# Optimization experiments

Measured on AMD Instinct MI355X. Metric: run time of the kernel, lower is better.

The kernel has to match this reference:

```python
import jax, jax.numpy as jnp
import numpy as np

N = 100_000        # PPI nodes
F_IN = 512         # num_features
H1, H2 = 16, 32    # GCN hidden / out channels
E = 3_200_000      # edges
NUM_DRUGS = 1024
B = 4096           # DDI batch rows


def setup_inputs() -> dict:
    key = jax.random.key(0)
    ks = jax.random.split(key, 16)
    s = 0.05
    return {
        "x": jax.random.normal(ks[0], (N, F_IN), jnp.float32),
        "edge_index": jax.random.randint(ks[1], (2, E), 0, N, dtype=jnp.int64),
        "DDI_feature": jax.random.normal(ks[2], (B, NUM_DRUGS + H2), jnp.float32),
        "W1": jax.random.normal(ks[3], (F_IN, H1), jnp.float32) * s,
        "b1": jax.random.normal(ks[4], (H1,), jnp.float32) * s,
        "W2": jax.random.normal(ks[5], (H1, H2), jnp.float32) * s,
        "b2": jax.random.normal(ks[6], (H2,), jnp.float32) * s,
        "fW1": jax.random.normal(ks[7], (NUM_DRUGS + H2, 64), jnp.float32) * s,
        "fb1": jax.random.normal(ks[8], (64,), jnp.float32) * s,
        "fW2": jax.random.normal(ks[9], (64, 16), jnp.float32) * s,
        "fb2": jax.random.normal(ks[10], (16,), jnp.float32) * s,
        "fW3": jax.random.normal(ks[11], (16, 1), jnp.float32) * s,
        "fb3": jax.random.normal(ks[12], (1,), jnp.float32) * s,
    }


def _gcn_conv(x, src, dst, W, b):
    """torch_geometric GCNConv with add_self_loops=True, symmetric norm.
    lin -> D^{-1/2} (A + I) D^{-1/2} -> + bias."""
    h = x @ W                                   # [N, out] linear first (faithful to GCNConv)
    ones = jnp.ones(src.shape[0], h.dtype)
    deg = jax.ops.segment_sum(ones, dst, num_segments=N) + 1.0  # +1 self-loop
    dinv = jax.lax.rsqrt(deg)                   # deg > 0 guaranteed by self-loop
    norm = dinv[src] * dinv[dst]                # [E]
    agg = jax.ops.segment_sum(h[src] * norm[:, None], dst, num_segments=N)
    agg = agg + h * (dinv * dinv)[:, None]      # self-loop message, norm = 1/deg
    return agg + b


def reference(x, edge_index, DDI_feature, W1, b1, W2, b2, fW1, fb1, fW2, fb2, fW3, fb3):
    src, dst = edge_index[0], edge_index[1]
    # PPI branch: conv1 -> relu -> (dropout: eval mode = identity) -> conv2 -> relu
    ppi = jax.nn.relu(_gcn_conv(x, src, dst, W1, b1))
    ppi = jax.nn.relu(_gcn_conv(ppi, src, dst, W2, b2))          # [N, 32]
    # DDI branch: fc1 -> relu -> fc2 -> relu -> fc3 -> relu
    ddi = jax.nn.relu(DDI_feature @ fW1 + fb1)
    ddi = jax.nn.relu(ddi @ fW2 + fb2)
    ddi = jax.nn.relu(ddi @ fW3 + fb3)                           # [B, 1]
    return ppi, ddi
```

## Files before the change

### kernel.cpp

```cpp
#include <hip/hip_runtime.h>

#define N_NODES 100000
#define HALF_N  50000
#define FEAT_IN 512
#define C1 16
#define C2 32
#define NEDGE 3200000
#define B_DDI 4096
#define F_DDI 1056

#define NBUCK 196
#define CAP_BUCK 32768
#define BIN_C 12288
#define NB_BIN ((NEDGE + BIN_C - 1) / BIN_C)
#define PB_CAP 12288

typedef float f4v __attribute__((ext_vector_type(4)));

#define O_DINV   0u
#define O_RP2    524288u
#define O_COL    1572864u
#define O_GBUF   16777216u
#define O_H1     46137344u
#define O_OUT1   54525952u
#define O_GCUR   71303168u
#define O_BBASE  71307264u


__global__ void k_ginit(int* __restrict__ gcur) {
    int i = threadIdx.x;
    if (i < NBUCK) gcur[i] = i * CAP_BUCK;
}

__global__ __launch_bounds__(256) void k_bin(const int* __restrict__ ei,
                                             int* __restrict__ gcur,
                                             unsigned int* __restrict__ gbuf) {
    __shared__ int lcnt[256];
    __shared__ int lscan[256];
    __shared__ int lbase[256];
    __shared__ unsigned int sdat[BIN_C];
    __shared__ unsigned char sb[BIN_C];
    int tid = threadIdx.x;
    int e0 = blockIdx.x * BIN_C;

    lcnt[tid] = 0;
    __syncthreads();
    #pragma unroll 4
    for (int j = 0; j < BIN_C / 256; ++j) {
        int e = e0 + j * 256 + tid;
        if (e < NEDGE) atomicAdd(&lcnt[ei[NEDGE + e] >> 9], 1);
    }
    __syncthreads();
    lscan[tid] = lcnt[tid];
    __syncthreads();
    for (int off = 1; off < 256; off <<= 1) {
        int t = (tid >= off) ? lscan[tid - off] : 0;
        __syncthreads();
        lscan[tid] += t;
        __syncthreads();
    }
    lscan[tid] -= lcnt[tid];
    if (tid < NBUCK) lbase[tid] = atomicAdd(&gcur[tid], lcnt[tid]);
    __syncthreads();
    lcnt[tid] = 0;
    __syncthreads();
    #pragma unroll 4
    for (int j = 0; j < BIN_C / 256; ++j) {
        int e = e0 + j * 256 + tid;
        if (e < NEDGE) {
            int s = ei[e];
            int d = ei[NEDGE + e];
            int b = d >> 9;
            int p = lscan[b] + atomicAdd(&lcnt[b], 1);
            sdat[p] = (unsigned int)s | ((unsigned int)(d & 511) << 17);
            sb[p] = (unsigned char)b;
        }
    }
    __syncthreads();
    int tot = (e0 + BIN_C <= NEDGE) ? BIN_C : (NEDGE - e0);
    for (int i = tid; i < tot; i += 256) {
        int b = sb[i];
        gbuf[lbase[b] + (i - lscan[b])] = sdat[i];
    }
}

__global__ void k_bbase(const int* __restrict__ gcur, int* __restrict__ bbase,
                        int* __restrict__ rp2) {
    __shared__ int s[256];
    int tid = threadIdx.x;
    int v = (tid < NBUCK) ? (gcur[tid] - tid * CAP_BUCK) : 0;
    s[tid] = v;
    __syncthreads();
    for (int off = 1; off < 256; off <<= 1) {
        int t = (tid >= off) ? s[tid - off] : 0;
        __syncthreads();
        s[tid] += t;
        __syncthreads();
    }
    if (tid < NBUCK) bbase[tid] = s[tid] - v;
    if (tid == 0) { bbase[NBUCK] = NEDGE; rp2[2 * N_NODES] = NEDGE; }
}

__global__ __launch_bounds__(512) void k_place(const int* __restrict__ bbase,
                                               const unsigned int* __restrict__ gbuf,
                                               int* __restrict__ col,
                                               int* __restrict__ rp2,
                                               float* __restrict__ dinv) {
    __shared__ int scat[PB_CAP];
    __shared__ int cnt2[1024];
    __shared__ int sc[512];
    __shared__ int lcur[1024];
    int b = blockIdx.x;
    int tid = threadIdx.x;
    int begc = bbase[b];
    int Eb = bbase[b + 1] - begc;
    const unsigned int* __restrict__ gb = gbuf + ((size_t)b << 15);
    int n0 = b * 512;

    cnt2[tid] = 0; cnt2[tid + 512] = 0;
    __syncthreads();
    for (int i = tid; i < Eb; i += 512) {
        unsigned int u = gb[i];
        int dl = (int)(u >> 17);
        int src = (int)(u & 0x1FFFFu);
        atomicAdd(&cnt2[dl * 2 + (src >= HALF_N)], 1);
    }
    __syncthreads();
    int a = cnt2[2 * tid], bb = cnt2[2 * tid + 1];
    sc[tid] = a + bb;
    __syncthreads();
    for (int off = 1; off < 512; off <<= 1) {
        int t = (tid >= off) ? sc[tid - off] : 0;
        __syncthreads();
        sc[tid] += t;
        __syncthreads();
    }
    int ex = sc[tid] - (a + bb);
    lcur[2 * tid] = ex;
    lcur[2 * tid + 1] = ex + a;
    int n = n0 + tid;
    if (n < N_NODES) {
        rp2[2 * n] = begc + ex;
        rp2[2 * n + 1] = begc + ex + a;
        dinv[n] = rsqrtf((float)(a + bb) + 1.0f);
    }
    __syncthreads();
    int h0 = sc[255];

    if (h0 <= PB_CAP && (Eb - h0) <= PB_CAP) {
        for (int i = tid; i < Eb; i += 512) {
            unsigned int u = gb[i];
            int dl = (int)(u >> 17);
            int src = (int)(u & 0x1FFFFu);
            if (dl < 256) {
                int p = atomicAdd(&lcur[dl * 2 + (src >= HALF_N)], 1);
                scat[p] = src;
            }
        }
        __syncthreads();
        for (int i = tid; i < h0; i += 512) col[begc + i] = scat[i];
        __syncthreads();
        for (int i = tid; i < Eb; i += 512) {
            unsigned int u = gb[i];
            int dl = (int)(u >> 17);
            int src = (int)(u & 0x1FFFFu);
            if (dl >= 256) {
                int p = atomicAdd(&lcur[dl * 2 + (src >= HALF_N)], 1);
                scat[p - h0] = src;
            }
        }
        __syncthreads();
        for (int i = tid; i < Eb - h0; i += 512) col[begc + h0 + i] = scat[i];
    } else {
        for (int i = tid; i < Eb; i += 512) {
            unsigned int u = gb[i];
            int dl = (int)(u >> 17);
            int src = (int)(u & 0x1FFFFu);
            int p = atomicAdd(&lcur[dl * 2 + (src >= HALF_N)], 1);
            col[begc + p] = src;
        }
    }
}


__global__ __launch_bounds__(256) void k_gemm1(const float* __restrict__ x,
                                               const float* __restrict__ W1,
                                               const float* __restrict__ dinv,
                                               float* __restrict__ h1s) {
    __shared__ float part[4][64][17];
    int tid = threadIdx.x;
    int wv = __builtin_amdgcn_readfirstlane(tid >> 6);
    int lane = tid & 63;
    int row = blockIdx.x * 64 + lane;
    int crow = row < N_NODES ? row : N_NODES - 1;
    const float* __restrict__ xr = x + (size_t)crow * FEAT_IN + wv * 128;

    float acc[16];
    #pragma unroll
    for (int c = 0; c < 16; ++c) acc[c] = 0.f;

    for (int it = 0; it < 8; ++it) {
        const float4* xp = reinterpret_cast<const float4*>(xr + it * 16);
        float4 xv0 = xp[0], xv1 = xp[1], xv2 = xp[2], xv3 = xp[3];
        float xs[16] = {xv0.x, xv0.y, xv0.z, xv0.w, xv1.x, xv1.y, xv1.z, xv1.w,
                        xv2.x, xv2.y, xv2.z, xv2.w, xv3.x, xv3.y, xv3.z, xv3.w};
        int kb = wv * 128 + it * 16;
        #pragma unroll
        for (int j = 0; j < 16; ++j) {
            const float* __restrict__ wr = W1 + (size_t)(kb + j) * 16;
            #pragma unroll
            for (int c = 0; c < 16; ++c) acc[c] = fmaf(xs[j], wr[c], acc[c]);
        }
    }
    #pragma unroll
    for (int c = 0; c < 16; ++c) part[wv][lane][c] = acc[c];
    __syncthreads();

    int r2 = tid >> 2, cq = tid & 3;
    int grow = blockIdx.x * 64 + r2;
    if (grow < N_NODES) {
        float dv = dinv[grow];
        float o[4];
        #pragma unroll
        for (int j = 0; j < 4; ++j) {
            int c = cq * 4 + j;
            o[j] = dv * (part[0][r2][c] + part[1][r2][c] + part[2][r2][c] + part[3][r2][c]);
        }
        *reinterpret_cast<float4*>(&h1s[(size_t)grow * C1 + cq * 4]) =
            make_float4(o[0], o[1], o[2], o[3]);
    }
}


__global__ __launch_bounds__(256) void k_gather1(const int* __restrict__ rp2, const int* __restrict__ col,
                                                 const float* __restrict__ dinv, const float* __restrict__ h1s,
                                                 const float* __restrict__ b1, float* __restrict__ out1s) {
    int t = blockIdx.x * 256 + threadIdx.x;
    int node = t >> 2;
    int q = t & 3;
    if (node >= N_NODES) return;
    int beg = rp2[2 * node], end = rp2[2 * node + 2];
    f4v acc = {0.f, 0.f, 0.f, 0.f};
    int p = beg;
    for (; p + 3 < end; p += 4) {
        int s0 = col[p], s1 = col[p + 1], s2 = col[p + 2], s3 = col[p + 3];
        f4v v0 = *reinterpret_cast<const f4v*>(&h1s[s0 * C1 + q * 4]);
        f4v v1 = *reinterpret_cast<const f4v*>(&h1s[s1 * C1 + q * 4]);
        f4v v2 = *reinterpret_cast<const f4v*>(&h1s[s2 * C1 + q * 4]);
        f4v v3 = *reinterpret_cast<const f4v*>(&h1s[s3 * C1 + q * 4]);
        acc += (v0 + v1) + (v2 + v3);
    }
    for (; p < end; ++p) {
        int s = col[p];
        acc += *reinterpret_cast<const f4v*>(&h1s[s * C1 + q * 4]);
    }
    float di = dinv[node];
    f4v hs = *reinterpret_cast<const f4v*>(&h1s[node * C1 + q * 4]);
    f4v bv = *reinterpret_cast<const f4v*>(&b1[q * 4]);
    f4v v = di * (acc + hs) + bv;
    f4v z = {0.f, 0.f, 0.f, 0.f};
    f4v r = v > z ? v : z;
    *reinterpret_cast<f4v*>(&out1s[node * C1 + q * 4]) = di * r;
}

__global__ __launch_bounds__(256) void k_gather2(const int* __restrict__ rp2, const int* __restrict__ col,
                                                 const float* __restrict__ dinv, const float* __restrict__ out1s,
                                                 const float* __restrict__ W2, const float* __restrict__ b2,
                                                 float* __restrict__ out) {
    __shared__ float sacc[64][17];
    __shared__ float sW[16 * 32];
    __shared__ float sb[32];
    int tid = threadIdx.x;
    if (tid < 128)
        *reinterpret_cast<float4*>(&sW[tid * 4]) = *reinterpret_cast<const float4*>(&W2[tid * 4]);
    if (tid < 32) sb[tid] = b2[tid];
    int g = tid >> 2;
    int q = tid & 3;
    int nodeRaw = blockIdx.x * 64 + g;
    int node = nodeRaw < N_NODES ? nodeRaw : N_NODES - 1;
    int beg = rp2[2 * node], end = rp2[2 * node + 2];
    f4v acc = {0.f, 0.f, 0.f, 0.f};
    int p = beg;
    for (; p + 3 < end; p += 4) {
        int s0 = col[p], s1 = col[p + 1], s2 = col[p + 2], s3 = col[p + 3];
        f4v v0 = *reinterpret_cast<const f4v*>(&out1s[s0 * C1 + q * 4]);
        f4v v1 = *reinterpret_cast<const f4v*>(&out1s[s1 * C1 + q * 4]);
        f4v v2 = *reinterpret_cast<const f4v*>(&out1s[s2 * C1 + q * 4]);
        f4v v3 = *reinterpret_cast<const f4v*>(&out1s[s3 * C1 + q * 4]);
        acc += (v0 + v1) + (v2 + v3);
    }
    for (; p < end; ++p) {
        int s = col[p];
        acc += *reinterpret_cast<const f4v*>(&out1s[s * C1 + q * 4]);
    }
    float di = dinv[node];
    f4v hs = *reinterpret_cast<const f4v*>(&out1s[node * C1 + q * 4]);
    f4v v = di * (acc + hs);
    sacc[g][q * 4 + 0] = v.x;
    sacc[g][q * 4 + 1] = v.y;
    sacc[g][q * 4 + 2] = v.z;
    sacc[g][q * 4 + 3] = v.w;
    __syncthreads();
    float r[8];
    #pragma unroll
    for (int j = 0; j < 8; ++j) r[j] = sb[q * 8 + j];
    #pragma unroll
    for (int k = 0; k < 16; ++k) {
        float a = sacc[g][k];
        const float* wrow = &sW[k * 32 + q * 8];
        #pragma unroll
        for (int j = 0; j < 8; ++j) r[j] = fmaf(a, wrow[j], r[j]);
    }
    if (nodeRaw < N_NODES) {
        f4v z = {0.f, 0.f, 0.f, 0.f};
        f4v o0 = {r[0], r[1], r[2], r[3]};
        f4v o1 = {r[4], r[5], r[6], r[7]};
        o0 = o0 > z ? o0 : z;
        o1 = o1 > z ? o1 : z;
        *reinterpret_cast<f4v*>(&out[nodeRaw * C2 + q * 8]) = o0;
        *reinterpret_cast<f4v*>(&out[nodeRaw * C2 + q * 8 + 4]) = o1;
    }
}


#define DDI_CHUNK 132

__global__ __launch_bounds__(256) void k_ddi(const float* __restrict__ feat,
                                             const float* __restrict__ fW1, const float* __restrict__ fb1,
                                             const float* __restrict__ fW2, const float* __restrict__ fb2,
                                             const float* __restrict__ fW3, const float* __restrict__ fb3,
                                             float* __restrict__ out) {
    __shared__ float sW[DDI_CHUNK * 64];
    __shared__ float sH[4][64];
    int tid = threadIdx.x;
    int wave = tid >> 6;
    int lane = tid & 63;
    int row = blockIdx.x * 4 + wave;

    float acc = 0.f;
    for (int k0 = 0; k0 < F_DDI; k0 += DDI_CHUNK) {
        __syncthreads();
        for (int idx = tid; idx < DDI_CHUNK * 64; idx += 256)
            sW[idx] = fW1[k0 * 64 + idx];
        __syncthreads();
        const float* frow = &feat[(size_t)row * F_DDI + k0];
        #pragma unroll 4
        for (int kk = 0; kk < DDI_CHUNK; kk += 4) {
            float4 fv = *reinterpret_cast<const float4*>(&frow[kk]);
            acc += fv.x * sW[(kk + 0) * 64 + lane];
            acc += fv.y * sW[(kk + 1) * 64 + lane];
            acc += fv.z * sW[(kk + 2) * 64 + lane];
            acc += fv.w * sW[(kk + 3) * 64 + lane];
        }
    }
    float h = fmaxf(acc + fb1[lane], 0.f);
    __syncthreads();
    sH[wave][lane] = h;
    __syncthreads();

    int c16 = lane & 15;
    float acc2 = 0.f;
    #pragma unroll
    for (int kk = 0; kk < 64; ++kk)
        acc2 += sH[wave][kk] * fW2[kk * 16 + c16];
    float o2 = fmaxf(acc2 + fb2[c16], 0.f);
    float part = o2 * fW3[c16];
    #pragma unroll
    for (int off = 8; off >= 1; off >>= 1)
        part += __shfl_xor(part, off, 16);
    if (lane == 0)
        out[row] = fmaxf(part + fb3[0], 0.f);
}


extern "C" void kernel_launch(void* const* d_in, const int* in_sizes, int n_in,
                              void* d_out, int out_size, void* d_ws, size_t ws_size,
                              hipStream_t stream) {
    const float* x   = (const float*)d_in[0];
    const int*   ei  = (const int*)d_in[1];
    const float* ddi = (const float*)d_in[2];
    const float* W1  = (const float*)d_in[3];
    const float* b1  = (const float*)d_in[4];
    const float* W2  = (const float*)d_in[5];
    const float* b2  = (const float*)d_in[6];
    const float* fW1 = (const float*)d_in[7];
    const float* fb1 = (const float*)d_in[8];
    const float* fW2 = (const float*)d_in[9];
    const float* fb2 = (const float*)d_in[10];
    const float* fW3 = (const float*)d_in[11];
    const float* fb3 = (const float*)d_in[12];

    char* ws = (char*)d_ws;
    float* dinv  = (float*)(ws + O_DINV);
    int*   rp2   = (int*)(ws + O_RP2);
    int*   col   = (int*)(ws + O_COL);
    unsigned int* gbuf = (unsigned int*)(ws + O_GBUF);
    float* h1s   = (float*)(ws + O_H1);
    float* out1s = (float*)(ws + O_OUT1);
    int*   gcur  = (int*)(ws + O_GCUR);
    int*   bbase = (int*)(ws + O_BBASE);

    float* out_ppi = (float*)d_out;
    float* out_ddi = out_ppi + (size_t)N_NODES * C2;

    k_ginit<<<1, 256, 0, stream>>>(gcur);
    k_bin<<<NB_BIN, 256, 0, stream>>>(ei, gcur, gbuf);
    k_bbase<<<1, 256, 0, stream>>>(gcur, bbase, rp2);
    k_place<<<NBUCK, 512, 0, stream>>>(bbase, gbuf, col, rp2, dinv);

    k_gemm1<<<(N_NODES + 63) / 64, 256, 0, stream>>>(x, W1, dinv, h1s);

    int gblk = (N_NODES * 4 + 255) / 256;
    k_gather1<<<gblk, 256, 0, stream>>>(rp2, col, dinv, h1s, b1, out1s);
    k_gather2<<<(N_NODES + 63) / 64, 256, 0, stream>>>(rp2, col, dinv, out1s, W2, b2, out_ppi);

    k_ddi<<<B_DDI / 4, 256, 0, stream>>>(ddi, fW1, fb1, fW2, fb2, fW3, fb3, out_ddi);
}
```

Before: 301.0 us.

## Fold bucket scan into placement, halve bin chunk, vectorize gather index loads

Drops the gcur init kernel and the separate bucket-base scan kernel. gcur is now zeroed with a memset, and every placement block recomputes the prefix scan over bucket counts itself. The binning chunk size is halved so more blocks run and each uses less shared memory. Both gather kernels now align the edge pointer and load column indices as int4 with an 8-way unrolled main loop, adding more loads in flight per thread at the cost of extra registers and a scalar prologue.

```diff
diff --git a/kernel.cpp b/kernel.cpp
--- a/kernel.cpp
+++ b/kernel.cpp
@@ -11,7 +11,7 @@
 
 #define NBUCK 196
 #define CAP_BUCK 32768
-#define BIN_C 12288
+#define BIN_C 6144
 #define NB_BIN ((NEDGE + BIN_C - 1) / BIN_C)
 #define PB_CAP 12288
 
@@ -24,13 +24,7 @@
 #define O_H1     46137344u
 #define O_OUT1   54525952u
 #define O_GCUR   71303168u
-#define O_BBASE  71307264u
-
-
-__global__ void k_ginit(int* __restrict__ gcur) {
-    int i = threadIdx.x;
-    if (i < NBUCK) gcur[i] = i * CAP_BUCK;
-}
+
 
 __global__ __launch_bounds__(256) void k_bin(const int* __restrict__ ei,
                                              int* __restrict__ gcur,
@@ -60,7 +54,7 @@
         __syncthreads();
     }
     lscan[tid] -= lcnt[tid];
-    if (tid < NBUCK) lbase[tid] = atomicAdd(&gcur[tid], lcnt[tid]);
+    if (tid < NBUCK) lbase[tid] = tid * CAP_BUCK + atomicAdd(&gcur[tid], lcnt[tid]);
     __syncthreads();
     lcnt[tid] = 0;
     __syncthreads();
@@ -84,36 +78,31 @@
     }
 }
 
-__global__ void k_bbase(const int* __restrict__ gcur, int* __restrict__ bbase,
-                        int* __restrict__ rp2) {
-    __shared__ int s[256];
-    int tid = threadIdx.x;
-    int v = (tid < NBUCK) ? (gcur[tid] - tid * CAP_BUCK) : 0;
-    s[tid] = v;
-    __syncthreads();
-    for (int off = 1; off < 256; off <<= 1) {
-        int t = (tid >= off) ? s[tid - off] : 0;
-        __syncthreads();
-        s[tid] += t;
-        __syncthreads();
-    }
-    if (tid < NBUCK) bbase[tid] = s[tid] - v;
-    if (tid == 0) { bbase[NBUCK] = NEDGE; rp2[2 * N_NODES] = NEDGE; }
-}
-
-__global__ __launch_bounds__(512) void k_place(const int* __restrict__ bbase,
+__global__ __launch_bounds__(512) void k_place(const int* __restrict__ gcur,
                                                const unsigned int* __restrict__ gbuf,
                                                int* __restrict__ col,
                                                int* __restrict__ rp2,
                                                float* __restrict__ dinv) {
     __shared__ int scat[PB_CAP];
+    __shared__ int pre[256];
     __shared__ int cnt2[1024];
     __shared__ int sc[512];
     __shared__ int lcur[1024];
     int b = blockIdx.x;
     int tid = threadIdx.x;
-    int begc = bbase[b];
-    int Eb = bbase[b + 1] - begc;
+
+    if (tid < 256) pre[tid] = (tid < NBUCK) ? gcur[tid] : 0;
+    __syncthreads();
+    for (int off = 1; off < 256; off <<= 1) {
+        int t = 0;
+        if (tid < 256 && tid >= off) t = pre[tid - off];
+        __syncthreads();
+        if (tid < 256) pre[tid] += t;
+        __syncthreads();
+    }
+    int Eb = gcur[b];
+    int begc = pre[b] - Eb;
+    if (b == NBUCK - 1 && tid == 0) rp2[2 * N_NODES] = NEDGE;
     const unsigned int* __restrict__ gb = gbuf + ((size_t)b << 15);
     int n0 = b * 512;
 
@@ -242,12 +231,29 @@
     int beg = rp2[2 * node], end = rp2[2 * node + 2];
     f4v acc = {0.f, 0.f, 0.f, 0.f};
     int p = beg;
+    while (p < end && (p & 3)) {
+        int s = col[p++];
+        acc += *reinterpret_cast<const f4v*>(&h1s[s * C1 + q * 4]);
+    }
+    for (; p + 7 < end; p += 8) {
+        int4 sa = *reinterpret_cast<const int4*>(&col[p]);
+        int4 sb = *reinterpret_cast<const int4*>(&col[p + 4]);
+        f4v v0 = *reinterpret_cast<const f4v*>(&h1s[sa.x * C1 + q * 4]);
+        f4v v1 = *reinterpret_cast<const f4v*>(&h1s[sa.y * C1 + q * 4]);
+        f4v v2 = *reinterpret_cast<const f4v*>(&h1s[sa.z * C1 + q * 4]);
+        f4v v3 = *reinterpret_cast<const f4v*>(&h1s[sa.w * C1 + q * 4]);
+        f4v v4 = *reinterpret_cast<const f4v*>(&h1s[sb.x * C1 + q * 4]);
+        f4v v5 = *reinterpret_cast<const f4v*>(&h1s[sb.y * C1 + q * 4]);
+        f4v v6 = *reinterpret_cast<const f4v*>(&h1s[sb.z * C1 + q * 4]);
+        f4v v7 = *reinterpret_cast<const f4v*>(&h1s[sb.w * C1 + q * 4]);
+        acc += ((v0 + v1) + (v2 + v3)) + ((v4 + v5) + (v6 + v7));
+    }
     for (; p + 3 < end; p += 4) {
-        int s0 = col[p], s1 = col[p + 1], s2 = col[p + 2], s3 = col[p + 3];
-        f4v v0 = *reinterpret_cast<const f4v*>(&h1s[s0 * C1 + q * 4]);
-        f4v v1 = *reinterpret_cast<const f4v*>(&h1s[s1 * C1 + q * 4]);
-        f4v v2 = *reinterpret_cast<const f4v*>(&h1s[s2 * C1 + q * 4]);
-        f4v v3 = *reinterpret_cast<const f4v*>(&h1s[s3 * C1 + q * 4]);
+        int4 sa = *reinterpret_cast<const int4*>(&col[p]);
+        f4v v0 = *reinterpret_cast<const f4v*>(&h1s[sa.x * C1 + q * 4]);
+        f4v v1 = *reinterpret_cast<const f4v*>(&h1s[sa.y * C1 + q * 4]);
+        f4v v2 = *reinterpret_cast<const f4v*>(&h1s[sa.z * C1 + q * 4]);
+        f4v v3 = *reinterpret_cast<const f4v*>(&h1s[sa.w * C1 + q * 4]);
         acc += (v0 + v1) + (v2 + v3);
     }
     for (; p < end; ++p) {
@@ -269,11 +275,11 @@
                                                  float* __restrict__ out) {
     __shared__ float sacc[64][17];
     __shared__ float sW[16 * 32];
-    __shared__ float sb[32];
+    __shared__ float sb2[32];
     int tid = threadIdx.x;
     if (tid < 128)
         *reinterpret_cast<float4*>(&sW[tid * 4]) = *reinterpret_cast<const float4*>(&W2[tid * 4]);
-    if (tid < 32) sb[tid] = b2[tid];
+    if (tid < 32) sb2[tid] = b2[tid];
     int g = tid >> 2;
     int q = tid & 3;
     int nodeRaw = blockIdx.x * 64 + g;
@@ -281,12 +287,29 @@
     int beg = rp2[2 * node], end = rp2[2 * node + 2];
     f4v acc = {0.f, 0.f, 0.f, 0.f};
     int p = beg;
+    while (p < end && (p & 3)) {
+        int s = col[p++];
+        acc += *reinterpret_cast<const f4v*>(&out1s[s * C1 + q * 4]);
+    }
+    for (; p + 7 < end; p += 8) {
+        int4 sa = *reinterpret_cast<const int4*>(&col[p]);
+        int4 sb = *reinterpret_cast<const int4*>(&col[p + 4]);
+        f4v v0 = *reinterpret_cast<const f4v*>(&out1s[sa.x * C1 + q * 4]);
+        f4v v1 = *reinterpret_cast<const f4v*>(&out1s[sa.y * C1 + q * 4]);
+        f4v v2 = *reinterpret_cast<const f4v*>(&out1s[sa.z * C1 + q * 4]);
+        f4v v3 = *reinterpret_cast<const f4v*>(&out1s[sa.w * C1 + q * 4]);
+        f4v v4 = *reinterpret_cast<const f4v*>(&out1s[sb.x * C1 + q * 4]);
+        f4v v5 = *reinterpret_cast<const f4v*>(&out1s[sb.y * C1 + q * 4]);
+        f4v v6 = *reinterpret_cast<const f4v*>(&out1s[sb.z * C1 + q * 4]);
+        f4v v7 = *reinterpret_cast<const f4v*>(&out1s[sb.w * C1 + q * 4]);
+        acc += ((v0 + v1) + (v2 + v3)) + ((v4 + v5) + (v6 + v7));
+    }
     for (; p + 3 < end; p += 4) {
-        int s0 = col[p], s1 = col[p + 1], s2 = col[p + 2], s3 = col[p + 3];
-        f4v v0 = *reinterpret_cast<const f4v*>(&out1s[s0 * C1 + q * 4]);
-        f4v v1 = *reinterpret_cast<const f4v*>(&out1s[s1 * C1 + q * 4]);
-        f4v v2 = *reinterpret_cast<const f4v*>(&out1s[s2 * C1 + q * 4]);
-        f4v v3 = *reinterpret_cast<const f4v*>(&out1s[s3 * C1 + q * 4]);
+        int4 sa = *reinterpret_cast<const int4*>(&col[p]);
+        f4v v0 = *reinterpret_cast<const f4v*>(&out1s[sa.x * C1 + q * 4]);
+        f4v v1 = *reinterpret_cast<const f4v*>(&out1s[sa.y * C1 + q * 4]);
+        f4v v2 = *reinterpret_cast<const f4v*>(&out1s[sa.z * C1 + q * 4]);
+        f4v v3 = *reinterpret_cast<const f4v*>(&out1s[sa.w * C1 + q * 4]);
         acc += (v0 + v1) + (v2 + v3);
     }
     for (; p < end; ++p) {
@@ -303,7 +326,7 @@
     __syncthreads();
     float r[8];
     #pragma unroll
-    for (int j = 0; j < 8; ++j) r[j] = sb[q * 8 + j];
+    for (int j = 0; j < 8; ++j) r[j] = sb2[q * 8 + j];
     #pragma unroll
     for (int k = 0; k < 16; ++k) {
         float a = sacc[g][k];
@@ -398,15 +421,13 @@
     float* h1s   = (float*)(ws + O_H1);
     float* out1s = (float*)(ws + O_OUT1);
     int*   gcur  = (int*)(ws + O_GCUR);
-    int*   bbase = (int*)(ws + O_BBASE);
 
     float* out_ppi = (float*)d_out;
     float* out_ddi = out_ppi + (size_t)N_NODES * C2;
 
-    k_ginit<<<1, 256, 0, stream>>>(gcur);
+    hipMemsetAsync(gcur, 0, NBUCK * sizeof(int), stream);
     k_bin<<<NB_BIN, 256, 0, stream>>>(ei, gcur, gbuf);
-    k_bbase<<<1, 256, 0, stream>>>(gcur, bbase, rp2);
-    k_place<<<NBUCK, 512, 0, stream>>>(bbase, gbuf, col, rp2, dinv);
+    k_place<<<NBUCK, 512, 0, stream>>>(gcur, gbuf, col, rp2, dinv);
 
     k_gemm1<<<(N_NODES + 63) / 64, 256, 0, stream>>>(x, W1, dinv, h1s);
 
```

Measured after the change: 282.0 us. -6.3%, faster.
